# Performance work log

Hardware: AMD Instinct MI355X
Metric: run time of the kernel (lower is better)

The kernel has to match this reference:

```python
import jax, jax.numpy as jnp
import numpy as np

D = 500  # hidden width hard-coded in the module

def _lrelu(x):
    # nn.LeakyReLU default negative_slope = 0.01
    return jnp.where(x > 0, x, 0.01 * x)

def setup_inputs() -> dict:
    key = jax.random.key(0)
    ks = jax.random.split(key, 20)
    T, B = 2048, 64
    inp = {
        "pitches": jax.random.normal(ks[0], (T, B, 128), dtype=jnp.float32),
        "velocities": jax.random.normal(ks[1], (T, B, 128), dtype=jnp.float32),
        "durations": jax.random.uniform(ks[2], (T, B, 1), dtype=jnp.float32),
        "steps": jax.random.uniform(ks[3], (T, B, 1), dtype=jnp.float32),
        # learned params (torch Linear convention: W is [out, in])
        "Wp": jax.random.normal(ks[4], (D, 128), dtype=jnp.float32) * 0.05,
        "bp": jax.random.normal(ks[5], (D,), dtype=jnp.float32) * 0.05,
        "Wv": jax.random.normal(ks[6], (D, 128), dtype=jnp.float32) * 0.05,
        "bv": jax.random.normal(ks[7], (D,), dtype=jnp.float32) * 0.05,
        "Wd": jax.random.normal(ks[8], (D, 1), dtype=jnp.float32) * 0.05,
        "bd": jax.random.normal(ks[9], (D,), dtype=jnp.float32) * 0.05,
        "Ws": jax.random.normal(ks[10], (D, 1), dtype=jnp.float32) * 0.05,
        "bs": jax.random.normal(ks[11], (D,), dtype=jnp.float32) * 0.05,
        "W1": jax.random.normal(ks[12], (D, D), dtype=jnp.float32) * 0.05,
        "b1": jax.random.normal(ks[13], (D,), dtype=jnp.float32) * 0.05,
        "W2": jax.random.normal(ks[14], (D, D), dtype=jnp.float32) * 0.05,
        "b2": jax.random.normal(ks[15], (D,), dtype=jnp.float32) * 0.05,
        "Wi": jax.random.normal(ks[16], (D, D), dtype=jnp.float32) * 0.05,
        "bi": jax.random.normal(ks[17], (D,), dtype=jnp.float32) * 0.05,
        "W3": jax.random.normal(ks[18], (1, D), dtype=jnp.float32) * 0.05,
        "b3": jax.random.normal(ks[19], (1,), dtype=jnp.float32) * 0.05,
    }
    return inp

def reference(pitches, velocities, durations, steps,
              Wp, bp, Wv, bv, Wd, bd, Ws, bs,
              W1, b1, W2, b2, Wi, bi, W3, b3):
    # Note: in the original torch code the LSTMCell output is computed then
    # discarded (overwritten), and `info` at step t depends only on inputs at
    # step t. Thus the final output depends only on the last timestep through
    # the embed-sum -> LeakyReLU MLP -> linear_intermediate chain.
    # Vectorized over all T timesteps (same per-step math as the loop body).
    add = (jnp.einsum('tbi,oi->tbo', pitches, Wp) + bp
           + jnp.einsum('tbi,oi->tbo', velocities, Wv) + bv
           + jnp.einsum('tbi,oi->tbo', durations, Wd) + bd
           + jnp.einsum('tbi,oi->tbo', steps, Ws) + bs)      # [T,B,500]
    h = _lrelu(jnp.einsum('tbi,oi->tbo', add, W1) + b1)
    h = _lrelu(jnp.einsum('tbi,oi->tbo', h, W2) + b2)
    info = jnp.einsum('tbi,oi->tbo', h, Wi) + bi              # [T,B,500]
    out = jax.nn.sigmoid(info[-1] @ W3.T + b3)                # [B,1]
    return out
```

## Files before the change

### kernel.cpp

```cpp
#include <hip/hip_runtime.h>

#define DD 500
#define BB 64
#define TT 2048
#define KP 128

__global__ __launch_bounds__(256) void k_embed_v(
    const float* __restrict__ pitches, const float* __restrict__ velocities,
    const float* __restrict__ durations, const float* __restrict__ steps,
    const float* __restrict__ Wp, const float* __restrict__ bp,
    const float* __restrict__ Wv, const float* __restrict__ bv,
    const float* __restrict__ Wd, const float* __restrict__ bd,
    const float* __restrict__ Wst, const float* __restrict__ bs,
    const float* __restrict__ Wi, const float* __restrict__ W3,
    float* __restrict__ addT, float* __restrict__ v)
{
    const int tid = threadIdx.x;
    const int bid = blockIdx.x;

    if (bid >= 125) {
        const int k = (bid - 125) * 256 + tid;
        if (k < DD) {
            float a0 = 0.f, a1 = 0.f, a2 = 0.f, a3 = 0.f;
            for (int o = 0; o < DD; o += 4) {
                a0 += W3[o + 0] * Wi[(o + 0) * DD + k];
                a1 += W3[o + 1] * Wi[(o + 1) * DD + k];
                a2 += W3[o + 2] * Wi[(o + 2) * DD + k];
                a3 += W3[o + 3] * Wi[(o + 3) * DD + k];
            }
            v[k] = (a0 + a1) + (a2 + a3);
        }
        return;
    }

    __shared__ float lds[KP * BB];
    const int b = tid & 63;
    const int o = __builtin_amdgcn_readfirstlane(bid * 4 + (tid >> 6));
    const float* __restrict__ wp = Wp + o * KP;
    const float* __restrict__ wv = Wv + o * KP;

    float a0 = 0.f, a1 = 0.f, a2 = 0.f, a3 = 0.f;

    const float4* Psrc = (const float4*)(pitches + (size_t)(TT - 1) * BB * KP);
    const float4* Vsrc = (const float4*)(velocities + (size_t)(TT - 1) * BB * KP);

    for (int j = tid; j < BB * KP / 4; j += 256) {
        float4 p = Psrc[j];
        int pb = j >> 5;
        int k0 = (j & 31) * 4;
        lds[(k0 + 0) * BB + ((pb + k0 + 0) & 63)] = p.x;
        lds[(k0 + 1) * BB + ((pb + k0 + 1) & 63)] = p.y;
        lds[(k0 + 2) * BB + ((pb + k0 + 2) & 63)] = p.z;
        lds[(k0 + 3) * BB + ((pb + k0 + 3) & 63)] = p.w;
    }
    __syncthreads();
    for (int k = 0; k < KP; k += 4) {
        a0 += lds[(k + 0) * BB + ((b + k + 0) & 63)] * wp[k + 0];
        a1 += lds[(k + 1) * BB + ((b + k + 1) & 63)] * wp[k + 1];
        a2 += lds[(k + 2) * BB + ((b + k + 2) & 63)] * wp[k + 2];
        a3 += lds[(k + 3) * BB + ((b + k + 3) & 63)] * wp[k + 3];
    }
    __syncthreads();

    for (int j = tid; j < BB * KP / 4; j += 256) {
        float4 p = Vsrc[j];
        int pb = j >> 5;
        int k0 = (j & 31) * 4;
        lds[(k0 + 0) * BB + ((pb + k0 + 0) & 63)] = p.x;
        lds[(k0 + 1) * BB + ((pb + k0 + 1) & 63)] = p.y;
        lds[(k0 + 2) * BB + ((pb + k0 + 2) & 63)] = p.z;
        lds[(k0 + 3) * BB + ((pb + k0 + 3) & 63)] = p.w;
    }
    __syncthreads();
    for (int k = 0; k < KP; k += 4) {
        a0 += lds[(k + 0) * BB + ((b + k + 0) & 63)] * wv[k + 0];
        a1 += lds[(k + 1) * BB + ((b + k + 1) & 63)] * wv[k + 1];
        a2 += lds[(k + 2) * BB + ((b + k + 2) & 63)] * wv[k + 2];
        a3 += lds[(k + 3) * BB + ((b + k + 3) & 63)] * wv[k + 3];
    }

    const float dur = durations[(size_t)(TT - 1) * BB + b];
    const float st  = steps[(size_t)(TT - 1) * BB + b];
    const float acc = bp[o] + bv[o] + bd[o] + bs[o]
                    + dur * Wd[o] + st * Wst[o]
                    + (a0 + a1) + (a2 + a3);
    addT[o * BB + b] = acc;
}

__global__ __launch_bounds__(256) void k_dense(
    const float* __restrict__ Ain, const float* __restrict__ W,
    const float* __restrict__ bias, float* __restrict__ Aout, int leaky)
{
    const int tid = threadIdx.x;
    const int b = tid & 63;
    const int o = __builtin_amdgcn_readfirstlane(blockIdx.x * 4 + (tid >> 6));
    const float* __restrict__ wrow = W + o * DD;

    float a0 = 0.f, a1 = 0.f, a2 = 0.f, a3 = 0.f;
    for (int k = 0; k < DD; k += 4) {
        a0 += Ain[(k + 0) * BB + b] * wrow[k + 0];
        a1 += Ain[(k + 1) * BB + b] * wrow[k + 1];
        a2 += Ain[(k + 2) * BB + b] * wrow[k + 2];
        a3 += Ain[(k + 3) * BB + b] * wrow[k + 3];
    }
    float acc = bias[o] + (a0 + a1) + (a2 + a3);
    if (leaky) acc = acc > 0.f ? acc : 0.01f * acc;
    Aout[o * BB + b] = acc;
}

__global__ __launch_bounds__(256) void k_out(
    const float* __restrict__ h2T, const float* __restrict__ v,
    const float* __restrict__ W3, const float* __restrict__ bi,
    const float* __restrict__ b3, float* __restrict__ out)
{
    __shared__ float partial[4][BB];
    const int tid = threadIdx.x;
    const int b = tid & 63;
    const int w = tid >> 6;
    const int kbeg = w * 125;

    float accA = 0.f, accB = 0.f;
    for (int k = kbeg; k < kbeg + 125; ++k) {
        accA += h2T[k * BB + b] * v[k];
        accB += W3[k] * bi[k];
    }
    partial[w][b] = accA + accB;
    __syncthreads();
    if (w == 0) {
        float s = partial[0][b] + partial[1][b] + partial[2][b] + partial[3][b]
                + b3[0];
        out[b] = 1.f / (1.f + __expf(-s));
    }
}

extern "C" void kernel_launch(void* const* d_in, const int* in_sizes, int n_in,
                              void* d_out, int out_size, void* d_ws, size_t ws_size,
                              hipStream_t stream)
{
    const float* pitches    = (const float*)d_in[0];
    const float* velocities = (const float*)d_in[1];
    const float* durations  = (const float*)d_in[2];
    const float* steps      = (const float*)d_in[3];
    const float* Wp  = (const float*)d_in[4];
    const float* bp  = (const float*)d_in[5];
    const float* Wv  = (const float*)d_in[6];
    const float* bv  = (const float*)d_in[7];
    const float* Wd  = (const float*)d_in[8];
    const float* bd  = (const float*)d_in[9];
    const float* Wst = (const float*)d_in[10];
    const float* bs  = (const float*)d_in[11];
    const float* W1  = (const float*)d_in[12];
    const float* b1  = (const float*)d_in[13];
    const float* W2  = (const float*)d_in[14];
    const float* b2  = (const float*)d_in[15];
    const float* Wi  = (const float*)d_in[16];
    const float* bi  = (const float*)d_in[17];
    const float* W3  = (const float*)d_in[18];
    const float* b3  = (const float*)d_in[19];

    float* ws   = (float*)d_ws;
    float* addT = ws;
    float* h1T  = ws + 32000;
    float* h2T  = ws + 64000;
    float* v    = ws + 96000;

    float* out = (float*)d_out;

    k_embed_v<<<127, 256, 0, stream>>>(pitches, velocities, durations, steps,
                                       Wp, bp, Wv, bv, Wd, bd, Wst, bs,
                                       Wi, W3, addT, v);
    k_dense<<<125, 256, 0, stream>>>(addT, W1, b1, h1T, 1);
    k_dense<<<125, 256, 0, stream>>>(h1T, W2, b2, h2T, 1);
    k_out<<<1, 256, 0, stream>>>(h2T, v, W3, bi, b3, out);
}
```

Baseline: 233.0 us.

## Split W3·Wi reduction across 32 blocks and widen dense-layer accumulators

Result: faster. 212.0 us (-9.0%).

```diff
diff --git a/kernel.cpp b/kernel.cpp
--- a/kernel.cpp
+++ b/kernel.cpp
@@ -4,6 +4,8 @@
 #define BB 64
 #define TT 2048
 #define KP 128
+#define VCHUNKS 32
+#define VPSTRIDE 512
 
 __global__ __launch_bounds__(256) void k_embed_v(
     const float* __restrict__ pitches, const float* __restrict__ velocities,
@@ -13,23 +15,27 @@
     const float* __restrict__ Wd, const float* __restrict__ bd,
     const float* __restrict__ Wst, const float* __restrict__ bs,
     const float* __restrict__ Wi, const float* __restrict__ W3,
-    float* __restrict__ addT, float* __restrict__ v)
+    float* __restrict__ addT, float* __restrict__ vpart)
 {
     const int tid = threadIdx.x;
     const int bid = blockIdx.x;
 
     if (bid >= 125) {
-        const int k = (bid - 125) * 256 + tid;
-        if (k < DD) {
-            float a0 = 0.f, a1 = 0.f, a2 = 0.f, a3 = 0.f;
-            for (int o = 0; o < DD; o += 4) {
-                a0 += W3[o + 0] * Wi[(o + 0) * DD + k];
-                a1 += W3[o + 1] * Wi[(o + 1) * DD + k];
-                a2 += W3[o + 2] * Wi[(o + 2) * DD + k];
-                a3 += W3[o + 3] * Wi[(o + 3) * DD + k];
-            }
-            v[k] = (a0 + a1) + (a2 + a3);
+        const int oc = bid - 125;
+        const int obeg = oc * 16;
+        const int k0 = tid;
+        const int k1 = tid + 256;
+        float acc0 = 0.f, acc1 = 0.f;
+        #pragma unroll
+        for (int i = 0; i < 16; ++i) {
+            const int o = obeg + i;
+            const int oc_ = o < DD ? o : DD - 1;
+            const float w = o < DD ? W3[oc_] : 0.f;
+            acc0 += w * Wi[(size_t)oc_ * DD + k0];
+            if (k1 < DD) acc1 += w * Wi[(size_t)oc_ * DD + k1];
         }
+        vpart[oc * VPSTRIDE + k0] = acc0;
+        if (k1 < DD) vpart[oc * VPSTRIDE + k1] = acc1;
         return;
     }
 
@@ -97,31 +103,56 @@
     const float* __restrict__ wrow = W + o * DD;
 
     float a0 = 0.f, a1 = 0.f, a2 = 0.f, a3 = 0.f;
-    for (int k = 0; k < DD; k += 4) {
+    float a4 = 0.f, a5 = 0.f, a6 = 0.f, a7 = 0.f;
+    for (int k = 0; k < 496; k += 8) {
         a0 += Ain[(k + 0) * BB + b] * wrow[k + 0];
         a1 += Ain[(k + 1) * BB + b] * wrow[k + 1];
         a2 += Ain[(k + 2) * BB + b] * wrow[k + 2];
         a3 += Ain[(k + 3) * BB + b] * wrow[k + 3];
-    }
-    float acc = bias[o] + (a0 + a1) + (a2 + a3);
+        a4 += Ain[(k + 4) * BB + b] * wrow[k + 4];
+        a5 += Ain[(k + 5) * BB + b] * wrow[k + 5];
+        a6 += Ain[(k + 6) * BB + b] * wrow[k + 6];
+        a7 += Ain[(k + 7) * BB + b] * wrow[k + 7];
+    }
+    a0 += Ain[496 * BB + b] * wrow[496];
+    a1 += Ain[497 * BB + b] * wrow[497];
+    a2 += Ain[498 * BB + b] * wrow[498];
+    a3 += Ain[499 * BB + b] * wrow[499];
+
+    float acc = bias[o] + ((a0 + a1) + (a2 + a3)) + ((a4 + a5) + (a6 + a7));
     if (leaky) acc = acc > 0.f ? acc : 0.01f * acc;
     Aout[o * BB + b] = acc;
 }
 
 __global__ __launch_bounds__(256) void k_out(
-    const float* __restrict__ h2T, const float* __restrict__ v,
+    const float* __restrict__ h2T, const float* __restrict__ vpart,
     const float* __restrict__ W3, const float* __restrict__ bi,
     const float* __restrict__ b3, float* __restrict__ out)
 {
+    __shared__ float vv[DD];
     __shared__ float partial[4][BB];
     const int tid = threadIdx.x;
+
+    for (int k = tid; k < DD; k += 256) {
+        float s0 = 0.f, s1 = 0.f, s2 = 0.f, s3 = 0.f;
+        #pragma unroll
+        for (int oc = 0; oc < VCHUNKS; oc += 4) {
+            s0 += vpart[(oc + 0) * VPSTRIDE + k];
+            s1 += vpart[(oc + 1) * VPSTRIDE + k];
+            s2 += vpart[(oc + 2) * VPSTRIDE + k];
+            s3 += vpart[(oc + 3) * VPSTRIDE + k];
+        }
+        vv[k] = (s0 + s1) + (s2 + s3);
+    }
+    __syncthreads();
+
     const int b = tid & 63;
     const int w = tid >> 6;
     const int kbeg = w * 125;
 
     float accA = 0.f, accB = 0.f;
     for (int k = kbeg; k < kbeg + 125; ++k) {
-        accA += h2T[k * BB + b] * v[k];
+        accA += h2T[k * BB + b] * vv[k];
         accB += W3[k] * bi[k];
     }
     partial[w][b] = accA + accB;
@@ -158,18 +189,18 @@
     const float* W3  = (const float*)d_in[18];
     const float* b3  = (const float*)d_in[19];
 
-    float* ws   = (float*)d_ws;
-    float* addT = ws;
-    float* h1T  = ws + 32000;
-    float* h2T  = ws + 64000;
-    float* v    = ws + 96000;
+    float* ws    = (float*)d_ws;
+    float* addT  = ws;
+    float* h1T   = ws + 32000;
+    float* h2T   = ws + 64000;
+    float* vpart = ws + 96000;
 
     float* out = (float*)d_out;
 
-    k_embed_v<<<127, 256, 0, stream>>>(pitches, velocities, durations, steps,
-                                       Wp, bp, Wv, bv, Wd, bd, Wst, bs,
-                                       Wi, W3, addT, v);
+    k_embed_v<<<125 + VCHUNKS, 256, 0, stream>>>(pitches, velocities, durations,
+                                                 steps, Wp, bp, Wv, bv, Wd, bd,
+                                                 Wst, bs, Wi, W3, addT, vpart);
     k_dense<<<125, 256, 0, stream>>>(addT, W1, b1, h1T, 1);
     k_dense<<<125, 256, 0, stream>>>(h1T, W2, b2, h2T, 1);
-    k_out<<<1, 256, 0, stream>>>(h2T, v, W3, bi, b3, out);
-}
+    k_out<<<1, 256, 0, stream>>>(h2T, vpart, W3, bi, b3, out);
+}
```
